# Kernel tuning notes

Measured on AMD Instinct MI355X. Metric: run time of the kernel, lower is better.

Reference implementation:

```python
import jax, jax.numpy as jnp
from jax import lax
import numpy as np

N, M, S = 16, 32, 128
ALPHA = 1e-06


def _conv(x, w, b, stride):
    y = lax.conv_general_dilated(x, w, (stride, stride), [(1, 1), (1, 1)],
                                 dimension_numbers=('NCHW', 'OIHW', 'NCHW'))
    return y + b[None, :, None, None]


def _deconv(x, w, b):
    # torch ConvTranspose2d(k=4, s=2, p=1); torch weight layout [in, out, kh, kw]
    k = jnp.transpose(w, (1, 0, 2, 3))[:, :, ::-1, ::-1]
    y = lax.conv_general_dilated(x, k, (1, 1), [(2, 2), (2, 2)],
                                 lhs_dilation=(2, 2),
                                 dimension_numbers=('NCHW', 'OIHW', 'NCHW'))
    return y + b[None, :, None, None]


def _kaiming(key, shape):
    fan_in = shape[1] * shape[2] * shape[3]
    return jax.random.normal(key, shape, dtype=jnp.float32) * np.float32(np.sqrt(2.0 / fan_in))


def setup_inputs():
    key = jax.random.key(0)
    ks = jax.random.split(key, 12)
    B, H, W = 8, 256, 256
    return {
        'x': jax.random.normal(ks[0], (B, 3, H, W), dtype=jnp.float32),
        'e0n_w1': _kaiming(ks[1], (N, 3, 3, 3)), 'e0n_b1': jnp.zeros((N,), jnp.float32),
        'e0n_w2': _kaiming(ks[2], (N, N, 3, 3)), 'e0n_b2': jnp.zeros((N,), jnp.float32),
        'e0s_w1': _kaiming(ks[3], (S, 3, 3, 3)), 'e0s_b1': jnp.zeros((S,), jnp.float32),
        'e0s_w2': _kaiming(ks[4], (S, S, 3, 3)), 'e0s_b2': jnp.zeros((S,), jnp.float32),
        'd0_dw': jax.random.normal(ks[5], (S, 3, 4, 4), jnp.float32) * np.float32(np.sqrt(2.0 / (3 * 16))),
        'd0_db': jnp.zeros((3,), jnp.float32),
        'd0_cw': _kaiming(ks[6], (3, 3, 3, 3)), 'd0_cb': jnp.zeros((3,), jnp.float32),
        'cell_k': jax.random.normal(ks[7], (M, N), jnp.float32) / np.float32(np.sqrt(N)),
        'cell_v': jax.random.normal(ks[8], (M, S), jnp.float32) / np.float32(np.sqrt(S)),
    }


def reference(x, e0n_w1, e0n_b1, e0n_w2, e0n_b2, e0s_w1, e0s_b1, e0s_w2, e0s_b2,
              d0_dw, d0_db, d0_cw, d0_cb, cell_k, cell_v):
    silu = jax.nn.silu
    # ConvBlock encoders (stride-2 on second conv)
    e0_n = silu(_conv(silu(_conv(x, e0n_w1, e0n_b1, 1)), e0n_w2, e0n_b2, 2))  # [B,N,H/2,W/2]
    e0_s = silu(_conv(silu(_conv(x, e0s_w1, e0s_b1, 1)), e0s_w2, e0s_b2, 2))  # [B,S,H/2,W/2]
    B, _, H, W = e0_n.shape
    # permute+flatten to token streams (the irregular-access glue)
    z = e0_n.transpose(0, 2, 3, 1).reshape(-1, N)        # [T, N]
    t_star = e0_s.transpose(0, 2, 3, 1).reshape(-1, S)   # [T, S]
    # memcell: softmax key/value retrieval over M slots
    w = jax.nn.softmax(z @ cell_k.T / jnp.sqrt(jnp.float32(N)), axis=-1)  # [T, M]
    t_hat = w @ cell_v                                   # read_update's read (old memory)
    cell_v_new = cell_v + ALPHA * (w.T @ (t_star - t_hat))  # delta-rule value update
    t_read = w @ cell_v_new                              # read(); d1_n == e0_n so weights reused
    d0_m = t_read.reshape(B, H, W, S).transpose(0, 3, 1, 2)  # [B,S,H/2,W/2]
    # DeconvBlock decoder back to 3 channels at full resolution
    d0_n = silu(_conv(silu(_deconv(d0_m, d0_dw, d0_db)), d0_cw, d0_cb, 1))
    return d0_n
```

## Files before the change

kernel.cpp:

```cpp
#include <hip/hip_runtime.h>
#include <hip/hip_bf16.h>


#define ALPHA_F 1e-6f

typedef __attribute__((ext_vector_type(8))) short bf16x8;
typedef __attribute__((ext_vector_type(4))) float f32x4;

__device__ __forceinline__ float silu_f(float x) {
    return x * __builtin_amdgcn_rcpf(1.f + __expf(-x));
}

__device__ __forceinline__ short f2bf(float f) {
    __hip_bfloat16 h = __float2bfloat16(f);
    union { __hip_bfloat16 b; short s; } u; u.b = h; return u.s;
}

__device__ __forceinline__ float bf2f(unsigned short s) {
    union { unsigned u; float f; } c; c.u = (unsigned)s << 16; return c.f;
}

__device__ __forceinline__ int pack_fp8x4(float a, float b, float c, float d) {
    int lo = __builtin_amdgcn_cvt_pk_fp8_f32(a, b, 0, false);
    return  __builtin_amdgcn_cvt_pk_fp8_f32(c, d, lo, true);
}

template<int CO>
__global__ __launch_bounds__(256) void conv1_silu(
    const float* __restrict__ x, const float* __restrict__ wgt,
    const float* __restrict__ bias, float* __restrict__ out)
{
    int idx = blockIdx.x * 256 + threadIdx.x;
    int w = idx & 255, h = (idx >> 8) & 255, b = idx >> 16;
    const float* xb = x + (size_t)b * 3 * 65536;
    float in[27];
#pragma unroll
    for (int ci = 0; ci < 3; ci++)
#pragma unroll
        for (int ky = 0; ky < 3; ky++)
#pragma unroll
            for (int kx = 0; kx < 3; kx++) {
                int hh = h + ky - 1, ww = w + kx - 1;
                bool ok = ((unsigned)hh < 256u) && ((unsigned)ww < 256u);
                in[(ci * 3 + ky) * 3 + kx] = ok ? xb[(ci << 16) + (hh << 8) + ww] : 0.f;
            }
    float* ob = out + (size_t)b * CO * 65536 + (h << 8) + w;
#pragma unroll 4
    for (int co = 0; co < CO; co++) {
        float acc = bias[co];
#pragma unroll
        for (int k = 0; k < 27; k++) acc += in[k] * wgt[co * 27 + k];
        ob[(size_t)co << 16] = silu_f(acc);
    }
}

#define C1K 40
__global__ __launch_bounds__(256) void conv1s_mfma(
    const float* __restrict__ x, const float* __restrict__ wgt,
    const float* __restrict__ bias, char* __restrict__ out8)
{
    __shared__ __align__(16) short Ps[128 * C1K];
    __shared__ __align__(16) short Ws[128 * C1K];
    int tid = threadIdx.x;
    int g = blockIdx.x;
    int b = g >> 9, rem = g & 511;
    int h = rem >> 1, w0 = (rem & 1) * 128;

    union { short s[32]; float4 v4[4]; } row;
#pragma unroll
    for (int k = 0; k < 32; k++) row.s[k] = 0;
    if (tid < 128) {
        int wpix = w0 + tid;
        const float* xb = x + (size_t)b * 3 * 65536;
#pragma unroll
        for (int ci = 0; ci < 3; ci++)
#pragma unroll
            for (int ky = 0; ky < 3; ky++)
#pragma unroll
                for (int kx = 0; kx < 3; kx++) {
                    int hh = h + ky - 1, ww = wpix + kx - 1;
                    float v = 0.f;
                    if (((unsigned)hh < 256u) && ((unsigned)ww < 256u))
                        v = xb[(ci << 16) + (hh << 8) + ww];
                    row.s[ci * 9 + ky * 3 + kx] = f2bf(v);
                }
#pragma unroll
        for (int j = 0; j < 4; j++) *(float4*)&Ps[tid * C1K + j * 8] = row.v4[j];
    } else {
        int co = tid - 128;
#pragma unroll
        for (int k = 0; k < 27; k++) row.s[k] = f2bf(wgt[co * 27 + k]);
#pragma unroll
        for (int j = 0; j < 4; j++) *(float4*)&Ws[co * C1K + j * 8] = row.v4[j];
    }
    __syncthreads();

    int lane = tid & 63, wave = tid >> 6;
    int coH = (wave & 1) * 64, pxH = (wave >> 1) * 64;
    int r16 = lane & 15, q = lane >> 4, koff = q * 8;
    bf16x8 af[4], bfr[4];
#pragma unroll
    for (int mt = 0; mt < 4; mt++)
        af[mt] = *(bf16x8*)&Ws[(coH + mt * 16 + r16) * C1K + koff];
#pragma unroll
    for (int nt = 0; nt < 4; nt++)
        bfr[nt] = *(bf16x8*)&Ps[(pxH + nt * 16 + r16) * C1K + koff];
    f32x4 acc[4][4];
#pragma unroll
    for (int mt = 0; mt < 4; mt++)
#pragma unroll
        for (int nt = 0; nt < 4; nt++) {
#pragma unroll
            for (int r = 0; r < 4; r++) acc[mt][nt][r] = 0.f;
            acc[mt][nt] = __builtin_amdgcn_mfma_f32_16x16x32_bf16(
                af[mt], bfr[nt], acc[mt][nt], 0, 0, 0);
        }

    int hwb = (h << 8) + w0 + pxH;
    int* ob4 = (int*)out8 + (size_t)b * 8 * 65536 * 4;
#pragma unroll
    for (int mt = 0; mt < 4; mt++) {
        int cb = coH + mt * 16 + q * 4;
        float4 bv = *(const float4*)&bias[cb];
        int cg = (coH + mt * 16) >> 4;
#pragma unroll
        for (int nt = 0; nt < 4; nt++) {
            int hw = hwb + nt * 16 + r16;
            int pk = pack_fp8x4(silu_f(acc[mt][nt][0] + bv.x),
                                silu_f(acc[mt][nt][1] + bv.y),
                                silu_f(acc[mt][nt][2] + bv.z),
                                silu_f(acc[mt][nt][3] + bv.w));
            ob4[((size_t)cg * 65536 + hw) * 4 + q] = pk;
        }
    }
}

__global__ __launch_bounds__(256) void wprep_kern(
    const float* __restrict__ w, int* __restrict__ wt8)
{
    int d = blockIdx.x * 256 + threadIdx.x;
    int pos = d >> 12;
    int rb = (d << 2) & 16383;
    int c16 = rb >> 11, co = (rb >> 4) & 127, e0 = rb & 15;
    float f[4];
#pragma unroll
    for (int j = 0; j < 4; j++) {
        int ci = c16 * 16 + e0 + j;
        f[j] = w[co * 1152 + ci * 9 + pos];
    }
    wt8[d] = pack_fp8x4(f[0], f[1], f[2], f[3]);
}

__global__ __launch_bounds__(256) void conv2s_mfma(
    const char* __restrict__ a8,
    const char* __restrict__ wt8,
    const float* __restrict__ bias, __hip_bfloat16* __restrict__ out)
{
    __shared__ __align__(16) char As[4 * 64 * 16];
    __shared__ __align__(16) char Bs[4 * 128 * 16];
    int tid = threadIdx.x;
    int g = blockIdx.x;
    int b = g >> 8, h2 = (g >> 1) & 127, w2base = (g & 1) * 64;
    int lane = tid & 63, wave = tid >> 6;
    int mrow = lane & 15, q = lane >> 4;

    f32x4 acc[2][4];
#pragma unroll
    for (int i = 0; i < 2; i++)
#pragma unroll
        for (int j = 0; j < 4; j++)
#pragma unroll
            for (int r = 0; r < 4; r++) acc[i][j][r] = 0.f;

    const float4* ab4 = (const float4*)a8 + (size_t)b * 8 * 65536;
    const float4* wb4 = (const float4*)wt8;
    int cA = tid >> 6, tokA = tid & 63;
    int sB0 = tid, sB1 = tid + 256;

#pragma unroll 1
    for (int pos = 0; pos < 9; pos++) {
        int ky = pos / 3, kx = pos - 3 * ky;
        int y = 2 * h2 - 1 + ky;
        if ((unsigned)y >= 256u) continue;
        int x = 2 * (w2base + tokA) - 1 + kx;
        int pix = (y << 8) + (x & 255);
#pragma unroll 1
        for (int cc = 0; cc < 2; cc++) {
            float4 a0 = make_float4(0.f, 0.f, 0.f, 0.f);
            if (x >= 0) a0 = ab4[(size_t)(cc * 4 + cA) * 65536 + pix];
            const float4* brow = wb4 + pos * 1024 + cc * 512;
            float4 b0 = brow[sB0], b1 = brow[sB1];
            __syncthreads();
            *(float4*)&As[tid * 16] = a0;
            *(float4*)&Bs[sB0 * 16] = b0;
            *(float4*)&Bs[sB1 * 16] = b1;
            __syncthreads();
#pragma unroll
            for (int kc = 0; kc < 2; kc++) {
                int cl = kc * 2 + (q >> 1), off = (q & 1) * 8;
                long afr[4], bfr[2];
#pragma unroll
                for (int mt = 0; mt < 4; mt++)
                    afr[mt] = *(long*)&As[(cl * 64 + mt * 16 + mrow) * 16 + off];
#pragma unroll
                for (int nt = 0; nt < 2; nt++)
                    bfr[nt] = *(long*)&Bs[(cl * 128 + wave * 32 + nt * 16 + mrow) * 16 + off];
#pragma unroll
                for (int nt = 0; nt < 2; nt++)
#pragma unroll
                    for (int mt = 0; mt < 4; mt++)
                        acc[nt][mt] = __builtin_amdgcn_mfma_f32_16x16x32_fp8_fp8(
                            afr[mt], bfr[nt], acc[nt][mt], 0, 0, 0);
            }
        }
    }
    int rowg = q * 4;
    size_t tbase = (size_t)g * 64;
#pragma unroll
    for (int nt = 0; nt < 2; nt++) {
        int co = wave * 32 + nt * 16 + mrow;
        float bvs = bias[co];
#pragma unroll
        for (int mt = 0; mt < 4; mt++)
#pragma unroll
            for (int r = 0; r < 4; r++) {
                int m = mt * 16 + rowg + r;
                out[(tbase + m) * 128 + co] =
                    __float2bfloat16(silu_f(acc[nt][mt][r] + bvs));
            }
    }
}

template<int CI, int CO>
__global__ __launch_bounds__(256) void conv2s2_silu(
    const float* __restrict__ in, const float* __restrict__ wgt,
    const float* __restrict__ bias, float* __restrict__ out)
{
    int idx = blockIdx.x * 256 + threadIdx.x;
    int w2 = idx & 127, h2 = (idx >> 7) & 127, b = idx >> 14;
    const float* ib = in + (size_t)b * CI * 65536;
    float acc[CO];
#pragma unroll
    for (int co = 0; co < CO; co++) acc[co] = bias[co];
    int h0 = 2 * h2 - 1, w0 = 2 * w2 - 1;
    for (int ci = 0; ci < CI; ci++) {
        float t[9];
#pragma unroll
        for (int ky = 0; ky < 3; ky++)
#pragma unroll
            for (int kx = 0; kx < 3; kx++) {
                int hh = h0 + ky, ww = w0 + kx;
                bool ok = ((unsigned)hh < 256u) && ((unsigned)ww < 256u);
                t[ky * 3 + kx] = ok ? ib[((size_t)ci << 16) + (hh << 8) + ww] : 0.f;
            }
#pragma unroll
        for (int co = 0; co < CO; co++)
#pragma unroll
            for (int k = 0; k < 9; k++)
                acc[co] += t[k] * wgt[(co * CI + ci) * 9 + k];
    }
    float* ob = out + (size_t)idx * CO;
#pragma unroll
    for (int co = 0; co < CO; co++) ob[co] = silu_f(acc[co]);
}

__global__ __launch_bounds__(256) void memcell_w_kern(
    const float* __restrict__ z, const float* __restrict__ ck, float* __restrict__ wout)
{
    int t = blockIdx.x * 256 + threadIdx.x;
    float zv[16];
    const float4* zp = (const float4*)(z + (size_t)t * 16);
#pragma unroll
    for (int i = 0; i < 4; i++) {
        float4 v = zp[i];
        zv[4 * i] = v.x; zv[4 * i + 1] = v.y; zv[4 * i + 2] = v.z; zv[4 * i + 3] = v.w;
    }
    float lg[32]; float mx = -1e30f;
#pragma unroll
    for (int m = 0; m < 32; m++) {
        float a = 0.f;
#pragma unroll
        for (int n = 0; n < 16; n++) a += zv[n] * ck[m * 16 + n];
        a *= 0.25f;
        lg[m] = a; mx = fmaxf(mx, a);
    }
    float s = 0.f;
#pragma unroll
    for (int m = 0; m < 32; m++) { lg[m] = __expf(lg[m] - mx); s += lg[m]; }
    float inv = 1.f / s;
    float4* wp = (float4*)(wout + (size_t)t * 32);
#pragma unroll
    for (int m = 0; m < 8; m++)
        wp[m] = make_float4(lg[4 * m] * inv, lg[4 * m + 1] * inv,
                            lg[4 * m + 2] * inv, lg[4 * m + 3] * inv);
}

__global__ __launch_bounds__(256) void memcell_acc_kern(
    const float* __restrict__ wmat, const __hip_bfloat16* __restrict__ tstar,
    float* __restrict__ part)
{
    __shared__ float ws[64][32];
    __shared__ float ts[64 * 128];
    int tid = threadIdx.x;
    int sg = tid & 31, mg = tid >> 5;
    int mW = tid & 31, m2 = (tid >> 5) * 4;
    float accT[16], accW[4];
#pragma unroll
    for (int i = 0; i < 16; i++) accT[i] = 0.f;
#pragma unroll
    for (int i = 0; i < 4; i++) accW[i] = 0.f;

#pragma unroll 1
    for (int cc = 0; cc < 2; cc++) {
        int c = blockIdx.x * 2 + cc;
        size_t base = (size_t)c * 64;
        __syncthreads();
        {
            const float4* src = (const float4*)(wmat + base * 32);
            float4* dst = (float4*)&ws[0][0];
#pragma unroll
            for (int i = 0; i < 2; i++) dst[tid + 256 * i] = src[tid + 256 * i];
            const float4* src2 = (const float4*)(tstar + base * 128);
#pragma unroll
            for (int i = 0; i < 4; i++) {
                union { float4 v; unsigned short us[8]; } u;
                u.v = src2[tid + 256 * i];
                float* d = &ts[(tid + 256 * i) * 8];
                float4 lo = make_float4(bf2f(u.us[0]), bf2f(u.us[1]), bf2f(u.us[2]), bf2f(u.us[3]));
                float4 hi = make_float4(bf2f(u.us[4]), bf2f(u.us[5]), bf2f(u.us[6]), bf2f(u.us[7]));
                *(float4*)d = lo; *(float4*)(d + 4) = hi;
            }
        }
        __syncthreads();
        for (int t = 0; t < 64; t++) {
            float4 wv = *(const float4*)&ws[t][mg * 4];
            float4 sv = *(const float4*)&ts[t * 128 + sg * 4];
            accT[0]  += wv.x * sv.x; accT[1]  += wv.x * sv.y; accT[2]  += wv.x * sv.z; accT[3]  += wv.x * sv.w;
            accT[4]  += wv.y * sv.x; accT[5]  += wv.y * sv.y; accT[6]  += wv.y * sv.z; accT[7]  += wv.y * sv.w;
            accT[8]  += wv.z * sv.x; accT[9]  += wv.z * sv.y; accT[10] += wv.z * sv.z; accT[11] += wv.z * sv.w;
            accT[12] += wv.w * sv.x; accT[13] += wv.w * sv.y; accT[14] += wv.w * sv.z; accT[15] += wv.w * sv.w;
            float wa = ws[t][mW];
            float4 wb = *(const float4*)&ws[t][m2];
            accW[0] += wa * wb.x; accW[1] += wa * wb.y;
            accW[2] += wa * wb.z; accW[3] += wa * wb.w;
        }
    }
    float* pb = part + (size_t)blockIdx.x * 5120;
#pragma unroll
    for (int i = 0; i < 16; i++) pb[i * 256 + tid] = accT[i];
#pragma unroll
    for (int i = 0; i < 4; i++) pb[4096 + i * 256 + tid] = accW[i];
}

__global__ __launch_bounds__(256) void memcell_reduce_kern(
    const float* __restrict__ part, float* __restrict__ WtT, float* __restrict__ WtW)
{
    int gid = blockIdx.x * 256 + threadIdx.x;
    int j = gid % 5120, seg = gid / 5120;
    const float* p = part + (size_t)seg * 64 * 5120 + j;
    float s = 0.f;
#pragma unroll 8
    for (int k = 0; k < 64; k++) s += p[(size_t)k * 5120];
    int i = j >> 8, t = j & 255;
    if (j < 4096) {
        int sg = t & 31, mg = t >> 5;
        atomicAdd(&WtT[(mg * 4 + (i >> 2)) * 128 + sg * 4 + (i & 3)], s);
    } else {
        int i2 = i - 16;
        int mW = t & 31, m2 = (t >> 5) * 4;
        atomicAdd(&WtW[mW * 32 + m2 + i2], s);
    }
}

__global__ __launch_bounds__(256) void cvnew_kern(
    const float* __restrict__ cv, const float* __restrict__ WtW,
    const float* __restrict__ WtT, float* __restrict__ cvn)
{
    int idx = blockIdx.x * 256 + threadIdx.x;
    int s = idx & 127, m = idx >> 7;
    float g = WtT[idx];
#pragma unroll
    for (int j = 0; j < 32; j++) g -= WtW[m * 32 + j] * cv[j * 128 + s];
    cvn[idx] = cv[idx] + ALPHA_F * g;
}

__global__ __launch_bounds__(256) void emat_kern(
    const float* __restrict__ cvn, const float* __restrict__ dw, float* __restrict__ E)
{
    int idx = blockIdx.x * 256 + threadIdx.x;
    int m = idx >> 6, j = idx & 63;
    int pos = j >> 2, co = j & 3;
    float s = 0.f;
    if (co < 3) {
        const float* cv = cvn + m * 128;
        for (int ci = 0; ci < 128; ci++)
            s += cv[ci] * dw[ci * 48 + co * 16 + pos];
    }
    E[idx] = s;
}

__global__ __launch_bounds__(256) void tread64_kern(
    const float* __restrict__ wmat, const float* __restrict__ E, float* __restrict__ t64)
{
    int t = blockIdx.x * 256 + threadIdx.x;
    float wv[32];
    const float4* wp = (const float4*)(wmat + (size_t)t * 32);
#pragma unroll
    for (int i = 0; i < 8; i++) {
        float4 v = wp[i];
        wv[4 * i] = v.x; wv[4 * i + 1] = v.y; wv[4 * i + 2] = v.z; wv[4 * i + 3] = v.w;
    }
    f32x4 acc[16];
#pragma unroll
    for (int i = 0; i < 16; i++)
#pragma unroll
        for (int r = 0; r < 4; r++) acc[i][r] = 0.f;
    const f32x4* E4 = (const f32x4*)E;
#pragma unroll 4
    for (int m = 0; m < 32; m++) {
        float wm = wv[m];
#pragma unroll
        for (int i = 0; i < 16; i++) {
            f32x4 e = E4[m * 16 + i];
#pragma unroll
            for (int r = 0; r < 4; r++) acc[i][r] += wm * e[r];
        }
    }
    f32x4* ob = (f32x4*)(t64 + (size_t)t * 64);
#pragma unroll
    for (int i = 0; i < 16; i++) ob[i] = acc[i];
}

__global__ __launch_bounds__(256) void dec_gather_kern(
    const float* __restrict__ t64, const float* __restrict__ db, float* __restrict__ out)
{
    int g = blockIdx.x;
    int wb = g & 7, hb = (g >> 3) & 7, b = g >> 6;
    int tx = threadIdx.x & 15, ty = threadIdx.x >> 4;
    int h2 = hb * 16 + ty, w2 = wb * 16 + tx;

    float mh[3], mw[3];
    int ihc[3], iwc[3];
#pragma unroll
    for (int a = 0; a < 3; a++) {
        int v = h2 - 1 + a;
        mh[a] = ((unsigned)v < 128u) ? 1.f : 0.f;
        ihc[a] = v < 0 ? 0 : (v > 127 ? 127 : v);
        v = w2 - 1 + a;
        mw[a] = ((unsigned)v < 128u) ? 1.f : 0.f;
        iwc[a] = v < 0 ? 0 : (v > 127 ? 127 : v);
    }
    float acc[2][2][3];
#pragma unroll
    for (int ph = 0; ph < 2; ph++)
#pragma unroll
        for (int pw = 0; pw < 2; pw++)
#pragma unroll
            for (int co = 0; co < 3; co++) acc[ph][pw][co] = db[co];

    const int RA[4] = {0, 1, 1, 2}, RP[4] = {0, 0, 1, 1}, RK[4] = {3, 1, 2, 0};
    const float* tb = t64 + (size_t)b * 16384 * 64;
#pragma unroll
    for (int ri = 0; ri < 4; ri++)
#pragma unroll
        for (int cj = 0; cj < 4; cj++) {
            int a = RA[ri], c = RA[cj];
            float m = mh[a] * mw[c];
            int tok = (ihc[a] << 7) + iwc[c];
            int pos = RK[ri] * 4 + RK[cj];
            float4 v = *(const float4*)&tb[(size_t)tok * 64 + pos * 4];
            int ph = RP[ri], pw = RP[cj];
            acc[ph][pw][0] += m * v.x;
            acc[ph][pw][1] += m * v.y;
            acc[ph][pw][2] += m * v.z;
        }
    int h = 2 * h2, w = 2 * w2;
#pragma unroll
    for (int ph = 0; ph < 2; ph++)
#pragma unroll
        for (int co = 0; co < 3; co++) {
            float2 v = make_float2(silu_f(acc[ph][0][co]), silu_f(acc[ph][1][co]));
            *(float2*)&out[(size_t)b * 3 * 65536 + (size_t)co * 65536 + ((size_t)(h + ph) << 8) + w] = v;
        }
}

extern "C" void kernel_launch(void* const* d_in, const int* in_sizes, int n_in,
                              void* d_out, int out_size, void* d_ws, size_t ws_size,
                              hipStream_t stream)
{
    const float* x      = (const float*)d_in[0];
    const float* e0n_w1 = (const float*)d_in[1];
    const float* e0n_b1 = (const float*)d_in[2];
    const float* e0n_w2 = (const float*)d_in[3];
    const float* e0n_b2 = (const float*)d_in[4];
    const float* e0s_w1 = (const float*)d_in[5];
    const float* e0s_b1 = (const float*)d_in[6];
    const float* e0s_w2 = (const float*)d_in[7];
    const float* e0s_b2 = (const float*)d_in[8];
    const float* d0_dw  = (const float*)d_in[9];
    const float* d0_db  = (const float*)d_in[10];
    const float* d0_cw  = (const float*)d_in[11];
    const float* d0_cb  = (const float*)d_in[12];
    const float* cell_k = (const float*)d_in[13];
    const float* cell_v = (const float*)d_in[14];
    float* outp = (float*)d_out;

    char* ws = (char*)d_ws;
    char* a_s8             = ws;
    __hip_bfloat16* t_star = (__hip_bfloat16*)(ws + 134217728);
    float* a_n    = (float*)(ws + 201326592);
    char* wt8     = (char*)(ws + 201326592);
    float* part   = (float*)(ws + 201850880);
    float* Emat   = (float*)(ws + 224000000);
    float* z      = (float*)(ws + 234881024);
    float* wmat   = (float*)(ws + 243269632);
    float* WtW    = (float*)(ws + 260046848);
    float* WtT    = (float*)(ws + 260050944);
    float* cvn    = (float*)(ws + 260067328);
    float* t64    = (float*)(ws);
    float* dec1   = (float*)(ws + 67108864);

    conv1_silu<16><<<2048, 256, 0, stream>>>(x, e0n_w1, e0n_b1, a_n);
    conv2s2_silu<16, 16><<<512, 256, 0, stream>>>(a_n, e0n_w2, e0n_b2, z);
    wprep_kern<<<144, 256, 0, stream>>>(e0s_w2, (int*)wt8);
    conv1s_mfma<<<4096, 256, 0, stream>>>(x, e0s_w1, e0s_b1, a_s8);
    conv2s_mfma<<<2048, 256, 0, stream>>>(a_s8, wt8, e0s_b2, t_star);
    memcell_w_kern<<<512, 256, 0, stream>>>(z, cell_k, wmat);
    hipMemsetAsync(WtW, 0, (1024 + 4096) * sizeof(float), stream);
    memcell_acc_kern<<<1024, 256, 0, stream>>>(wmat, t_star, part);
    memcell_reduce_kern<<<320, 256, 0, stream>>>(part, WtT, WtW);
    cvnew_kern<<<16, 256, 0, stream>>>(cell_v, WtW, WtT, cvn);
    emat_kern<<<8, 256, 0, stream>>>(cvn, d0_dw, Emat);
    tread64_kern<<<512, 256, 0, stream>>>(wmat, Emat, t64);
    dec_gather_kern<<<512, 256, 0, stream>>>(t64, d0_db, dec1);
    conv1_silu<3><<<2048, 256, 0, stream>>>(dec1, d0_cw, d0_cb, outp);
}
```

Baseline: 308.3 us.

## Fuse encoder conv2 with memcell softmax and split conv1s output channels across blocks

The stride-2 N-branch conv now computes the softmax key weights directly from its registers. This drops the intermediate z buffer and the separate memcell_w kernel launch. Separately, the MFMA conv1 for the S branch now gives each block 64 output channels instead of 128 and launches twice as many blocks. That halves per-wave accumulators and LDS use, which should raise parallelism, at the cost of recomputing the input patch im2col in both channel-half blocks.

```diff
diff --git a/kernel.cpp b/kernel.cpp
--- a/kernel.cpp
+++ b/kernel.cpp
@@ -60,11 +60,13 @@
     const float* __restrict__ bias, char* __restrict__ out8)
 {
     __shared__ __align__(16) short Ps[128 * C1K];
-    __shared__ __align__(16) short Ws[128 * C1K];
+    __shared__ __align__(16) short Ws[64 * C1K];
     int tid = threadIdx.x;
     int g = blockIdx.x;
-    int b = g >> 9, rem = g & 511;
-    int h = rem >> 1, w0 = (rem & 1) * 128;
+    int b = g >> 10, rem = g & 1023;
+    int hh2 = rem >> 1;
+    int h = hh2 >> 1, w0 = (hh2 & 1) * 128;
+    int coB = (rem & 1) * 64;
 
     union { short s[32]; float4 v4[4]; } row;
 #pragma unroll
@@ -78,36 +80,36 @@
             for (int ky = 0; ky < 3; ky++)
 #pragma unroll
                 for (int kx = 0; kx < 3; kx++) {
-                    int hh = h + ky - 1, ww = wpix + kx - 1;
+                    int hhp = h + ky - 1, ww = wpix + kx - 1;
                     float v = 0.f;
-                    if (((unsigned)hh < 256u) && ((unsigned)ww < 256u))
-                        v = xb[(ci << 16) + (hh << 8) + ww];
+                    if (((unsigned)hhp < 256u) && ((unsigned)ww < 256u))
+                        v = xb[(ci << 16) + (hhp << 8) + ww];
                     row.s[ci * 9 + ky * 3 + kx] = f2bf(v);
                 }
 #pragma unroll
         for (int j = 0; j < 4; j++) *(float4*)&Ps[tid * C1K + j * 8] = row.v4[j];
-    } else {
+    } else if (tid < 192) {
         int co = tid - 128;
 #pragma unroll
-        for (int k = 0; k < 27; k++) row.s[k] = f2bf(wgt[co * 27 + k]);
+        for (int k = 0; k < 27; k++) row.s[k] = f2bf(wgt[(coB + co) * 27 + k]);
 #pragma unroll
         for (int j = 0; j < 4; j++) *(float4*)&Ws[co * C1K + j * 8] = row.v4[j];
     }
     __syncthreads();
 
     int lane = tid & 63, wave = tid >> 6;
-    int coH = (wave & 1) * 64, pxH = (wave >> 1) * 64;
+    int coL = (wave & 1) * 32, pxH = (wave >> 1) * 64;
     int r16 = lane & 15, q = lane >> 4, koff = q * 8;
-    bf16x8 af[4], bfr[4];
-#pragma unroll
-    for (int mt = 0; mt < 4; mt++)
-        af[mt] = *(bf16x8*)&Ws[(coH + mt * 16 + r16) * C1K + koff];
+    bf16x8 af[2], bfr[4];
+#pragma unroll
+    for (int mt = 0; mt < 2; mt++)
+        af[mt] = *(bf16x8*)&Ws[(coL + mt * 16 + r16) * C1K + koff];
 #pragma unroll
     for (int nt = 0; nt < 4; nt++)
         bfr[nt] = *(bf16x8*)&Ps[(pxH + nt * 16 + r16) * C1K + koff];
-    f32x4 acc[4][4];
-#pragma unroll
-    for (int mt = 0; mt < 4; mt++)
+    f32x4 acc[2][4];
+#pragma unroll
+    for (int mt = 0; mt < 2; mt++)
 #pragma unroll
         for (int nt = 0; nt < 4; nt++) {
 #pragma unroll
@@ -119,10 +121,10 @@
     int hwb = (h << 8) + w0 + pxH;
     int* ob4 = (int*)out8 + (size_t)b * 8 * 65536 * 4;
 #pragma unroll
-    for (int mt = 0; mt < 4; mt++) {
-        int cb = coH + mt * 16 + q * 4;
+    for (int mt = 0; mt < 2; mt++) {
+        int cb = coB + coL + mt * 16 + q * 4;
         float4 bv = *(const float4*)&bias[cb];
-        int cg = (coH + mt * 16) >> 4;
+        int cg = (coB + coL + mt * 16) >> 4;
 #pragma unroll
         for (int nt = 0; nt < 4; nt++) {
             int hw = hwb + nt * 16 + r16;
@@ -231,19 +233,19 @@
     }
 }
 
-template<int CI, int CO>
-__global__ __launch_bounds__(256) void conv2s2_silu(
+__global__ __launch_bounds__(256) void conv2n_fused(
     const float* __restrict__ in, const float* __restrict__ wgt,
-    const float* __restrict__ bias, float* __restrict__ out)
+    const float* __restrict__ bias, const float* __restrict__ ck,
+    float* __restrict__ wout)
 {
     int idx = blockIdx.x * 256 + threadIdx.x;
     int w2 = idx & 127, h2 = (idx >> 7) & 127, b = idx >> 14;
-    const float* ib = in + (size_t)b * CI * 65536;
-    float acc[CO];
-#pragma unroll
-    for (int co = 0; co < CO; co++) acc[co] = bias[co];
+    const float* ib = in + (size_t)b * 16 * 65536;
+    float acc[16];
+#pragma unroll
+    for (int co = 0; co < 16; co++) acc[co] = bias[co];
     int h0 = 2 * h2 - 1, w0 = 2 * w2 - 1;
-    for (int ci = 0; ci < CI; ci++) {
+    for (int ci = 0; ci < 16; ci++) {
         float t[9];
 #pragma unroll
         for (int ky = 0; ky < 3; ky++)
@@ -254,27 +256,14 @@
                 t[ky * 3 + kx] = ok ? ib[((size_t)ci << 16) + (hh << 8) + ww] : 0.f;
             }
 #pragma unroll
-        for (int co = 0; co < CO; co++)
+        for (int co = 0; co < 16; co++)
 #pragma unroll
             for (int k = 0; k < 9; k++)
-                acc[co] += t[k] * wgt[(co * CI + ci) * 9 + k];
-    }
-    float* ob = out + (size_t)idx * CO;
-#pragma unroll
-    for (int co = 0; co < CO; co++) ob[co] = silu_f(acc[co]);
-}
-
-__global__ __launch_bounds__(256) void memcell_w_kern(
-    const float* __restrict__ z, const float* __restrict__ ck, float* __restrict__ wout)
-{
-    int t = blockIdx.x * 256 + threadIdx.x;
+                acc[co] += t[k] * wgt[(co * 16 + ci) * 9 + k];
+    }
     float zv[16];
-    const float4* zp = (const float4*)(z + (size_t)t * 16);
-#pragma unroll
-    for (int i = 0; i < 4; i++) {
-        float4 v = zp[i];
-        zv[4 * i] = v.x; zv[4 * i + 1] = v.y; zv[4 * i + 2] = v.z; zv[4 * i + 3] = v.w;
-    }
+#pragma unroll
+    for (int co = 0; co < 16; co++) zv[co] = silu_f(acc[co]);
     float lg[32]; float mx = -1e30f;
 #pragma unroll
     for (int m = 0; m < 32; m++) {
@@ -288,7 +277,7 @@
 #pragma unroll
     for (int m = 0; m < 32; m++) { lg[m] = __expf(lg[m] - mx); s += lg[m]; }
     float inv = 1.f / s;
-    float4* wp = (float4*)(wout + (size_t)t * 32);
+    float4* wp = (float4*)(wout + (size_t)idx * 32);
 #pragma unroll
     for (int m = 0; m < 8; m++)
         wp[m] = make_float4(lg[4 * m] * inv, lg[4 * m + 1] * inv,
@@ -512,7 +501,6 @@
     char* wt8     = (char*)(ws + 201326592);
     float* part   = (float*)(ws + 201850880);
     float* Emat   = (float*)(ws + 224000000);
-    float* z      = (float*)(ws + 234881024);
     float* wmat   = (float*)(ws + 243269632);
     float* WtW    = (float*)(ws + 260046848);
     float* WtT    = (float*)(ws + 260050944);
@@ -521,11 +509,10 @@
     float* dec1   = (float*)(ws + 67108864);
 
     conv1_silu<16><<<2048, 256, 0, stream>>>(x, e0n_w1, e0n_b1, a_n);
-    conv2s2_silu<16, 16><<<512, 256, 0, stream>>>(a_n, e0n_w2, e0n_b2, z);
+    conv2n_fused<<<512, 256, 0, stream>>>(a_n, e0n_w2, e0n_b2, cell_k, wmat);
     wprep_kern<<<144, 256, 0, stream>>>(e0s_w2, (int*)wt8);
-    conv1s_mfma<<<4096, 256, 0, stream>>>(x, e0s_w1, e0s_b1, a_s8);
+    conv1s_mfma<<<8192, 256, 0, stream>>>(x, e0s_w1, e0s_b1, a_s8);
     conv2s_mfma<<<2048, 256, 0, stream>>>(a_s8, wt8, e0s_b2, t_star);
-    memcell_w_kern<<<512, 256, 0, stream>>>(z, cell_k, wmat);
     hipMemsetAsync(WtW, 0, (1024 + 4096) * sizeof(float), stream);
     memcell_acc_kern<<<1024, 256, 0, stream>>>(wmat, t_star, part);
     memcell_reduce_kern<<<320, 256, 0, stream>>>(part, WtT, WtW);
```

Result: no change. 305.2 us (-1.0%).
